# Optimization experiments

Measured on AMD Instinct MI355X. Metric: run time of the kernel, lower is better.

Reference implementation:

```python
import jax, jax.numpy as jnp
import numpy as np

N = 6144
D = 128
TAU = 0.1
ADJ_P = 0.005  # edge density


def _l2_normalize(x, eps=1e-12):
    # matches torch F.normalize: x / max(||x||, eps)
    n = jnp.sqrt(jnp.sum(x * x, axis=-1, keepdims=True))
    return x / jnp.maximum(n, eps)


def setup_inputs() -> dict:
    key = jax.random.key(0)
    ks = jax.random.split(key, 8)
    embF = jax.random.normal(ks[0], (N, D), jnp.float32)
    embM = jax.random.normal(ks[1], (N, D), jnp.float32)
    embP = jax.random.normal(ks[2], (N, D), jnp.float32)
    FM_adj = (jax.random.uniform(ks[3], (N, N)) < ADJ_P).astype(jnp.float32)
    FP_adj = (jax.random.uniform(ks[4], (N, N)) < ADJ_P).astype(jnp.float32)
    W1 = jax.random.normal(ks[5], (2 * D, D), jnp.float32) * (1.0 / np.sqrt(2 * D))
    b1 = jnp.zeros((D,), jnp.float32)
    W2 = jax.random.normal(ks[6], (D, 2), jnp.float32) * (1.0 / np.sqrt(D))
    b2 = jnp.zeros((2,), jnp.float32)
    return {"embF": embF, "embM": embM, "embP": embP,
            "FM_adj": FM_adj, "FP_adj": FP_adj,
            "W1": W1, "b1": b1, "W2": W2, "b2": b2}


def reference(embF, embM, embP, FM_adj, FP_adj, W1, b1, W2, b2):
    # attention-weighted neighbor aggregation
    FM_repr = (FM_adj @ embM) / jnp.maximum(FM_adj.sum(1, keepdims=True), 1.0)
    FP_repr = (FP_adj @ embP) / jnp.maximum(FP_adj.sum(1, keepdims=True), 1.0)
    # stack(dim=1).view(N,-1) == concat along feature dim
    feat = jnp.concatenate([FM_repr, FP_repr], axis=1)            # [N, 2D]
    h = jnp.maximum(feat @ W1 + b1, 0.0)                           # ReLU (dropout inactive in eval)
    weights = jax.nn.softmax(h @ W2 + b2, axis=-1)                 # [N, 2]

    Fn = _l2_normalize(embF)
    Mn = _l2_normalize(embM)
    Pn = _l2_normalize(embP)

    FM_sim = jnp.exp((Fn @ Mn.T) / TAU)                            # [N, Nm]
    FP_sim = jnp.exp((Fn @ Pn.T) / TAU)                            # [N, Np]

    FM_pos = jnp.sum(FM_sim * FM_adj, axis=1)
    FP_pos = jnp.sum(FP_sim * FP_adj, axis=1)
    FM_neg = jnp.sum(FM_sim, axis=1) - FM_pos
    FP_neg = jnp.sum(FP_sim, axis=1) - FP_pos

    w0, w1w = weights[:, 0], weights[:, 1]
    wp = w0 * FM_pos + w1w * FP_pos
    wn = w0 * FM_neg + w1w * FP_neg

    nei_count = jnp.maximum(FM_adj.sum(1) + FP_adj.sum(1), 1.0)
    ratio = wp / (wp + wn) / nei_count
    ratio = jnp.maximum(ratio, 1e-10)
    loss = jnp.mean(-jnp.log(ratio))
    return loss, weights
```

## Files before the change

### kernel.cpp

```cpp
#include <hip/hip_runtime.h>
#include <hip/hip_bf16.h>

#define NN 6144
#define DD 128
#define PBL 136
#define INV_TAU 10.0f

typedef __attribute__((ext_vector_type(4))) float f32x4;
typedef __attribute__((ext_vector_type(8))) short s16x8;

__global__ void k_normalize(const float* __restrict__ embF,
                            const float* __restrict__ embM,
                            const float* __restrict__ embP,
                            float* __restrict__ Fn,
                            float* __restrict__ rnM, float* __restrict__ rnP,
                            __hip_bfloat16* __restrict__ Fnb,
                            __hip_bfloat16* __restrict__ Mnb,
                            __hip_bfloat16* __restrict__ Pnb) {
    int which = blockIdx.y;
    const float* src = which == 0 ? embF : (which == 1 ? embM : embP);
    __hip_bfloat16* dstb = which == 0 ? Fnb : (which == 1 ? Mnb : Pnb);
    int wave = threadIdx.x >> 6, lane = threadIdx.x & 63;
    int row = blockIdx.x * 4 + wave;
    float2 v = reinterpret_cast<const float2*>(src + (size_t)row * DD)[lane];
    float s = v.x * v.x + v.y * v.y;
#pragma unroll
    for (int m = 1; m <= 32; m <<= 1) s += __shfl_xor(s, m);
    float inv = 1.0f / fmaxf(sqrtf(s), 1e-12f);
    float2 o; o.x = v.x * inv; o.y = v.y * inv;
    if (which == 0)
        reinterpret_cast<float2*>(Fn + (size_t)row * DD)[lane] = o;
    if (lane == 0) {
        if (which == 1) rnM[row] = inv;
        if (which == 2) rnP[row] = inv;
    }
    __hip_bfloat162 ob;
    ob.x = __float2bfloat16(o.x);
    ob.y = __float2bfloat16(o.y);
    reinterpret_cast<__hip_bfloat162*>(dstb + (size_t)row * DD)[lane] = ob;
}

__global__ __launch_bounds__(256) void k_scan(
        const float* __restrict__ FM_adj, const float* __restrict__ FP_adj,
        int* __restrict__ nzbuf, int* __restrict__ nzcnt,
        float* __restrict__ cntF, float* __restrict__ cntP) {
    __shared__ int lbuf[4][64 * 12];
    const int h = blockIdx.y;
    const float* adj = h ? FP_adj : FM_adj;
    const int w = threadIdx.x >> 6, lane = threadIdx.x & 63;
    const int row = blockIdx.x * 4 + w;
    const float4* rp = reinterpret_cast<const float4*>(adj + (size_t)row * NN);
    int* mybuf = &lbuf[w][lane * 12];
    int mycnt = 0;
    for (int b = 0; b < 3; ++b) {
        const int c0 = b * 8 * 64 + lane;
        float4 v0 = rp[c0];
        float4 v1 = rp[c0 + 64];
        float4 v2 = rp[c0 + 128];
        float4 v3 = rp[c0 + 192];
        float4 v4 = rp[c0 + 256];
        float4 v5 = rp[c0 + 320];
        float4 v6 = rp[c0 + 384];
        float4 v7 = rp[c0 + 448];
        float4 vv[8] = {v0, v1, v2, v3, v4, v5, v6, v7};
#pragma unroll
        for (int u = 0; u < 8; ++u) {
            int colbase = (b * 8 + u) * 256 + lane * 4;
            if (vv[u].x != 0.f) { if (mycnt < 12) mybuf[mycnt] = colbase;     mycnt++; }
            if (vv[u].y != 0.f) { if (mycnt < 12) mybuf[mycnt] = colbase + 1; mycnt++; }
            if (vv[u].z != 0.f) { if (mycnt < 12) mybuf[mycnt] = colbase + 2; mycnt++; }
            if (vv[u].w != 0.f) { if (mycnt < 12) mybuf[mycnt] = colbase + 3; mycnt++; }
        }
    }
    int cnt = mycnt < 12 ? mycnt : 12;
    int x = cnt;
#pragma unroll
    for (int d = 1; d < 64; d <<= 1) {
        int y = __shfl_up(x, d);
        if (lane >= d) x += y;
    }
    int pref = x - cnt;
    int totc = __shfl(x, 63);
    int t = mycnt;
#pragma unroll
    for (int msk = 1; msk <= 32; msk <<= 1) t += __shfl_xor(t, msk);
    const int base = (h * NN + row) << 7;
    for (int i = 0; i < cnt; ++i) {
        int slot = pref + i;
        if (slot < 128) nzbuf[base + slot] = mybuf[i];
    }
    if (lane == 0) {
        nzcnt[h * NN + row] = totc < 128 ? totc : 128;
        (h ? cntP : cntF)[row] = (float)t;
    }
}

__global__ __launch_bounds__(256) void k_dense(
        const __hip_bfloat16* __restrict__ Fnb,
        const __hip_bfloat16* __restrict__ Mnb,
        const __hip_bfloat16* __restrict__ Pnb,
        float* __restrict__ FMtot, float* __restrict__ FPtot) {
    __shared__ __hip_bfloat16 Bs[32][PBL];
    const int half = blockIdx.z;
    const __hip_bfloat16* Bnb = half ? Pnb : Mnb;
    float* TOT = half ? FPtot : FMtot;
    const int tid = threadIdx.x;
    const int w = tid >> 6, lane = tid & 63;
    const int m = lane & 15, q = lane >> 4;
    const int rb = blockIdx.x * 128 + w * 32;
    const int j0 = blockIdx.y * (NN / 8);
    const int srow = tid >> 4, scol = (tid & 15) * 8;

    s16x8 a[2][4];
#pragma unroll
    for (int g = 0; g < 2; ++g)
#pragma unroll
        for (int ks = 0; ks < 4; ++ks)
            a[g][ks] = *reinterpret_cast<const s16x8*>(
                Fnb + (size_t)(rb + g * 16 + m) * DD + ks * 32 + q * 8);

    const float4* gt0 = reinterpret_cast<const float4*>(Bnb + (size_t)j0 * DD);
    float4 s0 = gt0[tid], s1 = gt0[256 + tid];

    float tot[2][4] = {{0.f, 0.f, 0.f, 0.f}, {0.f, 0.f, 0.f, 0.f}};
    for (int it = 0; it < 24; ++it) {
        __syncthreads();
        *reinterpret_cast<float4*>(&Bs[srow][scol]) = s0;
        *reinterpret_cast<float4*>(&Bs[16 + srow][scol]) = s1;
        __syncthreads();
        if (it + 1 < 24) {
            const float4* gt = reinterpret_cast<const float4*>(
                Bnb + (size_t)(j0 + (it + 1) * 32) * DD);
            s0 = gt[tid];
            s1 = gt[256 + tid];
        }
        asm volatile("" ::: "memory");
        s16x8 b[2][4];
#pragma unroll
        for (int t = 0; t < 2; ++t)
#pragma unroll
            for (int ks = 0; ks < 4; ++ks)
                b[t][ks] = *reinterpret_cast<const s16x8*>(
                    &Bs[t * 16 + m][ks * 32 + q * 8]);
#pragma unroll
        for (int g = 0; g < 2; ++g)
#pragma unroll
            for (int t = 0; t < 2; ++t) {
                f32x4 acc = {0.f, 0.f, 0.f, 0.f};
#pragma unroll
                for (int ks = 0; ks < 4; ++ks)
                    acc = __builtin_amdgcn_mfma_f32_16x16x32_bf16(
                        a[g][ks], b[t][ks], acc, 0, 0, 0);
#pragma unroll
                for (int r = 0; r < 4; ++r)
                    tot[g][r] += __expf(acc[r] * INV_TAU);
            }
    }
#pragma unroll
    for (int msk = 1; msk <= 8; msk <<= 1)
#pragma unroll
        for (int g = 0; g < 2; ++g)
#pragma unroll
            for (int r = 0; r < 4; ++r)
                tot[g][r] += __shfl_xor(tot[g][r], msk);
    if (m == 0)
#pragma unroll
        for (int g = 0; g < 2; ++g)
#pragma unroll
            for (int r = 0; r < 4; ++r)
                atomicAdd(&TOT[rb + g * 16 + q * 4 + r], tot[g][r]);
}

__global__ void k_gather(const float* __restrict__ embM,
                         const float* __restrict__ embP,
                         const float* __restrict__ Fn,
                         const float* __restrict__ rnM,
                         const float* __restrict__ rnP,
                         const int* __restrict__ nzbuf,
                         const int* __restrict__ nzcnt,
                         const float* __restrict__ cntF,
                         const float* __restrict__ cntP,
                         float* __restrict__ feat,
                         float* __restrict__ FMpos, float* __restrict__ FPpos) {
    __shared__ int listS[128];
    __shared__ float rS[2][DD];
    __shared__ float posS[2];
    const int row = blockIdx.x, h = blockIdx.y;
    const int tid = threadIdx.x, wv = tid >> 6, lane = tid & 63;
    const float* embX = h ? embP : embM;
    const float* RN = h ? rnP : rnM;
    int K = nzcnt[h * NN + row];
    if (tid < K) listS[tid] = nzbuf[((h * NN + row) << 7) + tid];
    __syncthreads();
    float2 f = reinterpret_cast<const float2*>(Fn + (size_t)row * DD)[lane];
    float2 racc = {0.f, 0.f};
    float wsum = 0.f;
    for (int k = wv; k < K; k += 2) {
        int j = listS[k];
        float rn = RN[j];
        float2 e = reinterpret_cast<const float2*>(embX + (size_t)j * DD)[lane];
        racc.x += e.x;
        racc.y += e.y;
        float d = f.x * e.x + f.y * e.y;
#pragma unroll
        for (int msk = 1; msk <= 32; msk <<= 1) d += __shfl_xor(d, msk);
        wsum += __expf(d * rn * INV_TAU);
    }
    rS[wv][2 * lane] = racc.x;
    rS[wv][2 * lane + 1] = racc.y;
    if (lane == 0) posS[wv] = wsum;
    __syncthreads();
    float cn = (h ? cntP : cntF)[row];
    feat[(size_t)row * (2 * DD) + h * DD + tid] =
        (rS[0][tid] + rS[1][tid]) / fmaxf(cn, 1.0f);
    if (tid == 0) (h ? FPpos : FMpos)[row] = posS[0] + posS[1];
}

__global__ __launch_bounds__(256) void k_mlp(
        const float* __restrict__ feat,
        const float* __restrict__ W1, const float* __restrict__ b1,
        const float* __restrict__ W2, const float* __restrict__ b2,
        const float* __restrict__ FMpos, const float* __restrict__ FPpos,
        const float* __restrict__ FMtot, const float* __restrict__ FPtot,
        const float* __restrict__ cntF, const float* __restrict__ cntP,
        float* __restrict__ out) {
    __shared__ float featS[8][2 * DD];
    __shared__ float red[4][4][2];
    __shared__ float lossS[8];
    const int tid = threadIdx.x;
    const int g = tid >> 7, d = tid & 127;
    const int wv = tid >> 6, lane = tid & 63;
    const int row0 = blockIdx.x * 8;
    for (int idx = tid; idx < 8 * 2 * DD; idx += 256)
        featS[idx >> 8][idx & 255] = feat[(size_t)row0 * (2 * DD) + idx];
    __syncthreads();
    float bb = b1[d];
    float acc0 = bb, acc1 = bb, acc2 = bb, acc3 = bb;
    const float* fS = &featS[g * 4][0];
#pragma unroll 4
    for (int c = 0; c < 2 * DD; ++c) {
        float w1v = W1[c * DD + d];
        acc0 = fmaf(fS[0 * 256 + c], w1v, acc0);
        acc1 = fmaf(fS[1 * 256 + c], w1v, acc1);
        acc2 = fmaf(fS[2 * 256 + c], w1v, acc2);
        acc3 = fmaf(fS[3 * 256 + c], w1v, acc3);
    }
    float w20 = W2[2 * d], w21 = W2[2 * d + 1];
    float hr[4] = {fmaxf(acc0, 0.f), fmaxf(acc1, 0.f),
                   fmaxf(acc2, 0.f), fmaxf(acc3, 0.f)};
#pragma unroll
    for (int r = 0; r < 4; ++r) {
        float p0 = hr[r] * w20, p1 = hr[r] * w21;
#pragma unroll
        for (int msk = 1; msk <= 32; msk <<= 1) {
            p0 += __shfl_xor(p0, msk);
            p1 += __shfl_xor(p1, msk);
        }
        if (lane == 0) { red[wv][r][0] = p0; red[wv][r][1] = p1; }
    }
    __syncthreads();
    if (tid < 8) {
        int g2 = tid >> 2, r = tid & 3;
        int row = row0 + tid;
        float z0 = red[2 * g2][r][0] + red[2 * g2 + 1][r][0] + b2[0];
        float z1 = red[2 * g2][r][1] + red[2 * g2 + 1][r][1] + b2[1];
        float mx = fmaxf(z0, z1);
        float e0 = expf(z0 - mx), e1 = expf(z1 - mx);
        float inv = 1.0f / (e0 + e1);
        float w0 = e0 * inv, w1 = e1 * inv;
        out[1 + row * 2 + 0] = w0;
        out[1 + row * 2 + 1] = w1;
        float wp = w0 * FMpos[row] + w1 * FPpos[row];
        float wn = w0 * (FMtot[row] - FMpos[row]) +
                   w1 * (FPtot[row] - FPpos[row]);
        float nei = fmaxf(cntF[row] + cntP[row], 1.0f);
        float ratio = wp / (wp + wn) / nei;
        ratio = fmaxf(ratio, 1e-10f);
        lossS[tid] = -logf(ratio);
    }
    __syncthreads();
    if (tid == 0) {
        float L = 0.f;
#pragma unroll
        for (int r = 0; r < 8; ++r) L += lossS[r];
        atomicAdd(out, L * (1.0f / NN));
    }
}

extern "C" void kernel_launch(void* const* d_in, const int* in_sizes, int n_in,
                              void* d_out, int out_size, void* d_ws, size_t ws_size,
                              hipStream_t stream) {
    const float* embF   = (const float*)d_in[0];
    const float* embM   = (const float*)d_in[1];
    const float* embP   = (const float*)d_in[2];
    const float* FM_adj = (const float*)d_in[3];
    const float* FP_adj = (const float*)d_in[4];
    const float* W1     = (const float*)d_in[5];
    const float* b1     = (const float*)d_in[6];
    const float* W2     = (const float*)d_in[7];
    const float* b2     = (const float*)d_in[8];
    float* out = (float*)d_out;

    float* ws = (float*)d_ws;
    float* FMtot = ws;
    float* FPtot = FMtot + NN;
    float* FMpos = FPtot + NN;
    float* FPpos = FMpos + NN;
    float* cntF  = FPpos + NN;
    float* cntP  = cntF + NN;
    float* rnM   = cntP + NN;
    float* rnP   = rnM + NN;
    float* feat  = rnP + NN;
    float* Fn    = feat + (size_t)NN * 2 * DD;
    __hip_bfloat16* Fnb = (__hip_bfloat16*)(Fn + (size_t)NN * DD);
    __hip_bfloat16* Mnb = Fnb + (size_t)NN * DD;
    __hip_bfloat16* Pnb = Mnb + (size_t)NN * DD;
    int* nzbuf = (int*)(Pnb + (size_t)NN * DD);
    int* nzcnt = nzbuf + 2 * (size_t)NN * 128;

    hipMemsetAsync(FMtot, 0, 2 * NN * sizeof(float), stream);
    hipMemsetAsync(d_out, 0, sizeof(float), stream);

    k_normalize<<<dim3(NN / 4, 3), 256, 0, stream>>>(embF, embM, embP,
                                                     Fn, rnM, rnP,
                                                     Fnb, Mnb, Pnb);
    k_scan<<<dim3(NN / 4, 2), 256, 0, stream>>>(FM_adj, FP_adj,
                                                nzbuf, nzcnt, cntF, cntP);
    k_dense<<<dim3(NN / 128, 8, 2), 256, 0, stream>>>(Fnb, Mnb, Pnb,
                                                      FMtot, FPtot);
    k_gather<<<dim3(NN, 2), 128, 0, stream>>>(embM, embP, Fn, rnM, rnP,
                                              nzbuf, nzcnt, cntF, cntP,
                                              feat, FMpos, FPpos);
    k_mlp<<<dim3(NN / 8), 256, 0, stream>>>(feat, W1, b1, W2, b2,
                                            FMpos, FPpos, FMtot, FPtot,
                                            cntF, cntP, out);
}
```

Measured before the change: 449.9 us.

## Fuse adjacency scan with sparse gather, split dense grid finer, retile MLP

Merges the adjacency scan and the neighbor gather into one kernel with one block per row, so the nonzero index list stays in shared memory and the global nzbuf round trip and one launch go away. The dense similarity kernel's column split is doubled (16 chunks of 12 iterations) to give more blocks and parallelism, at the cost of more atomics. The MLP kernel is reorganised so each thread handles 8 rows over half the input channels, with a shared-memory reduction. Per-thread nonzero capacity drops from 12 to 4 entries, which relies on the sparse adjacency density.

```diff
diff --git a/kernel.cpp b/kernel.cpp
--- a/kernel.cpp
+++ b/kernel.cpp
@@ -40,58 +40,101 @@
     reinterpret_cast<__hip_bfloat162*>(dstb + (size_t)row * DD)[lane] = ob;
 }
 
-__global__ __launch_bounds__(256) void k_scan(
+__global__ __launch_bounds__(256) void k_sparse2(
         const float* __restrict__ FM_adj, const float* __restrict__ FP_adj,
-        int* __restrict__ nzbuf, int* __restrict__ nzcnt,
+        const float* __restrict__ embM, const float* __restrict__ embP,
+        const float* __restrict__ Fn,
+        const float* __restrict__ rnM, const float* __restrict__ rnP,
+        float* __restrict__ feat,
+        float* __restrict__ FMpos, float* __restrict__ FPpos,
         float* __restrict__ cntF, float* __restrict__ cntP) {
-    __shared__ int lbuf[4][64 * 12];
-    const int h = blockIdx.y;
-    const float* adj = h ? FP_adj : FM_adj;
-    const int w = threadIdx.x >> 6, lane = threadIdx.x & 63;
-    const int row = blockIdx.x * 4 + w;
+    __shared__ float FnS[DD];
+    __shared__ int lbufT[256][4];
+    __shared__ int listS[128];
+    __shared__ float reprS[8][DD];
+    __shared__ float posS[8];
+    __shared__ int wvS[4];
+    __shared__ int Ktot[2];
+    const int row = blockIdx.x, h = blockIdx.y;
+    const float* adj  = h ? FP_adj : FM_adj;
+    const float* embX = h ? embP : embM;
+    const float* RN   = h ? rnP : rnM;
+    const int tid = threadIdx.x, wv = tid >> 6, lane = tid & 63;
+
+    if (tid < 32)
+        reinterpret_cast<float4*>(FnS)[tid] =
+            reinterpret_cast<const float4*>(Fn + (size_t)row * DD)[tid];
+
     const float4* rp = reinterpret_cast<const float4*>(adj + (size_t)row * NN);
-    int* mybuf = &lbuf[w][lane * 12];
     int mycnt = 0;
-    for (int b = 0; b < 3; ++b) {
-        const int c0 = b * 8 * 64 + lane;
-        float4 v0 = rp[c0];
-        float4 v1 = rp[c0 + 64];
-        float4 v2 = rp[c0 + 128];
-        float4 v3 = rp[c0 + 192];
-        float4 v4 = rp[c0 + 256];
-        float4 v5 = rp[c0 + 320];
-        float4 v6 = rp[c0 + 384];
-        float4 v7 = rp[c0 + 448];
-        float4 vv[8] = {v0, v1, v2, v3, v4, v5, v6, v7};
-#pragma unroll
-        for (int u = 0; u < 8; ++u) {
-            int colbase = (b * 8 + u) * 256 + lane * 4;
-            if (vv[u].x != 0.f) { if (mycnt < 12) mybuf[mycnt] = colbase;     mycnt++; }
-            if (vv[u].y != 0.f) { if (mycnt < 12) mybuf[mycnt] = colbase + 1; mycnt++; }
-            if (vv[u].z != 0.f) { if (mycnt < 12) mybuf[mycnt] = colbase + 2; mycnt++; }
-            if (vv[u].w != 0.f) { if (mycnt < 12) mybuf[mycnt] = colbase + 3; mycnt++; }
-        }
-    }
-    int cnt = mycnt < 12 ? mycnt : 12;
+#pragma unroll
+    for (int it = 0; it < 6; ++it) {
+        float4 v = rp[it * 256 + tid];
+        int cb = (it * 256 + tid) * 4;
+        if (v.x != 0.f) { if (mycnt < 4) lbufT[tid][mycnt] = cb;     mycnt++; }
+        if (v.y != 0.f) { if (mycnt < 4) lbufT[tid][mycnt] = cb + 1; mycnt++; }
+        if (v.z != 0.f) { if (mycnt < 4) lbufT[tid][mycnt] = cb + 2; mycnt++; }
+        if (v.w != 0.f) { if (mycnt < 4) lbufT[tid][mycnt] = cb + 3; mycnt++; }
+    }
+    int cnt = mycnt < 4 ? mycnt : 4;
     int x = cnt;
 #pragma unroll
     for (int d = 1; d < 64; d <<= 1) {
         int y = __shfl_up(x, d);
         if (lane >= d) x += y;
     }
-    int pref = x - cnt;
-    int totc = __shfl(x, 63);
     int t = mycnt;
 #pragma unroll
     for (int msk = 1; msk <= 32; msk <<= 1) t += __shfl_xor(t, msk);
-    const int base = (h * NN + row) << 7;
+    if (tid == 0) Ktot[1] = 0;
+    if (lane == 63) wvS[wv] = x;
+    __syncthreads();
+    if (lane == 0) atomicAdd(&Ktot[1], t);
+    if (tid == 0) {
+        int s = 0;
+#pragma unroll
+        for (int i = 0; i < 4; ++i) { int v = wvS[i]; wvS[i] = s; s += v; }
+        Ktot[0] = s < 128 ? s : 128;
+    }
+    __syncthreads();
+    int off = wvS[wv] + (x - cnt);
     for (int i = 0; i < cnt; ++i) {
-        int slot = pref + i;
-        if (slot < 128) nzbuf[base + slot] = mybuf[i];
-    }
-    if (lane == 0) {
-        nzcnt[h * NN + row] = totc < 128 ? totc : 128;
-        (h ? cntP : cntF)[row] = (float)t;
+        int s = off + i;
+        if (s < 128) listS[s] = lbufT[tid][i];
+    }
+    __syncthreads();
+    const int K = Ktot[0];
+    const float trueK = (float)Ktot[1];
+
+    const int hw = tid >> 5, sl = tid & 31;
+    float4 f4 = reinterpret_cast<const float4*>(FnS)[sl];
+    float4 racc = {0.f, 0.f, 0.f, 0.f};
+    float wsum = 0.f;
+    for (int k = hw; k < K; k += 8) {
+        int j = listS[k];
+        float rn = RN[j];
+        float4 e = reinterpret_cast<const float4*>(embX + (size_t)j * DD)[sl];
+        racc.x += e.x; racc.y += e.y; racc.z += e.z; racc.w += e.w;
+        float d = f4.x * e.x + f4.y * e.y + f4.z * e.z + f4.w * e.w;
+#pragma unroll
+        for (int msk = 1; msk <= 16; msk <<= 1) d += __shfl_xor(d, msk);
+        wsum += __expf(d * rn * INV_TAU);
+    }
+    reinterpret_cast<float4*>(&reprS[hw][0])[sl] = racc;
+    if (sl == 0) posS[hw] = wsum;
+    __syncthreads();
+    if (tid < DD) {
+        float s = 0.f;
+#pragma unroll
+        for (int i = 0; i < 8; ++i) s += reprS[i][tid];
+        feat[(size_t)row * (2 * DD) + h * DD + tid] = s / fmaxf(trueK, 1.0f);
+    }
+    if (tid == 0) {
+        float p = 0.f;
+#pragma unroll
+        for (int i = 0; i < 8; ++i) p += posS[i];
+        (h ? FPpos : FMpos)[row] = p;
+        (h ? cntP : cntF)[row] = trueK;
     }
 }
 
@@ -108,7 +151,7 @@
     const int w = tid >> 6, lane = tid & 63;
     const int m = lane & 15, q = lane >> 4;
     const int rb = blockIdx.x * 128 + w * 32;
-    const int j0 = blockIdx.y * (NN / 8);
+    const int j0 = blockIdx.y * (NN / 16);
     const int srow = tid >> 4, scol = (tid & 15) * 8;
 
     s16x8 a[2][4];
@@ -123,12 +166,12 @@
     float4 s0 = gt0[tid], s1 = gt0[256 + tid];
 
     float tot[2][4] = {{0.f, 0.f, 0.f, 0.f}, {0.f, 0.f, 0.f, 0.f}};
-    for (int it = 0; it < 24; ++it) {
+    for (int it = 0; it < 12; ++it) {
         __syncthreads();
         *reinterpret_cast<float4*>(&Bs[srow][scol]) = s0;
         *reinterpret_cast<float4*>(&Bs[16 + srow][scol]) = s1;
         __syncthreads();
-        if (it + 1 < 24) {
+        if (it + 1 < 12) {
             const float4* gt = reinterpret_cast<const float4*>(
                 Bnb + (size_t)(j0 + (it + 1) * 32) * DD);
             s0 = gt[tid];
@@ -169,51 +212,6 @@
 #pragma unroll
             for (int r = 0; r < 4; ++r)
                 atomicAdd(&TOT[rb + g * 16 + q * 4 + r], tot[g][r]);
-}
-
-__global__ void k_gather(const float* __restrict__ embM,
-                         const float* __restrict__ embP,
-                         const float* __restrict__ Fn,
-                         const float* __restrict__ rnM,
-                         const float* __restrict__ rnP,
-                         const int* __restrict__ nzbuf,
-                         const int* __restrict__ nzcnt,
-                         const float* __restrict__ cntF,
-                         const float* __restrict__ cntP,
-                         float* __restrict__ feat,
-                         float* __restrict__ FMpos, float* __restrict__ FPpos) {
-    __shared__ int listS[128];
-    __shared__ float rS[2][DD];
-    __shared__ float posS[2];
-    const int row = blockIdx.x, h = blockIdx.y;
-    const int tid = threadIdx.x, wv = tid >> 6, lane = tid & 63;
-    const float* embX = h ? embP : embM;
-    const float* RN = h ? rnP : rnM;
-    int K = nzcnt[h * NN + row];
-    if (tid < K) listS[tid] = nzbuf[((h * NN + row) << 7) + tid];
-    __syncthreads();
-    float2 f = reinterpret_cast<const float2*>(Fn + (size_t)row * DD)[lane];
-    float2 racc = {0.f, 0.f};
-    float wsum = 0.f;
-    for (int k = wv; k < K; k += 2) {
-        int j = listS[k];
-        float rn = RN[j];
-        float2 e = reinterpret_cast<const float2*>(embX + (size_t)j * DD)[lane];
-        racc.x += e.x;
-        racc.y += e.y;
-        float d = f.x * e.x + f.y * e.y;
-#pragma unroll
-        for (int msk = 1; msk <= 32; msk <<= 1) d += __shfl_xor(d, msk);
-        wsum += __expf(d * rn * INV_TAU);
-    }
-    rS[wv][2 * lane] = racc.x;
-    rS[wv][2 * lane + 1] = racc.y;
-    if (lane == 0) posS[wv] = wsum;
-    __syncthreads();
-    float cn = (h ? cntP : cntF)[row];
-    feat[(size_t)row * (2 * DD) + h * DD + tid] =
-        (rS[0][tid] + rS[1][tid]) / fmaxf(cn, 1.0f);
-    if (tid == 0) (h ? FPpos : FMpos)[row] = posS[0] + posS[1];
 }
 
 __global__ __launch_bounds__(256) void k_mlp(
@@ -225,45 +223,59 @@
         const float* __restrict__ cntF, const float* __restrict__ cntP,
         float* __restrict__ out) {
     __shared__ float featS[8][2 * DD];
-    __shared__ float red[4][4][2];
+    __shared__ float partS[2][8][DD];
+    __shared__ float redS[2][8][2];
     __shared__ float lossS[8];
     const int tid = threadIdx.x;
-    const int g = tid >> 7, d = tid & 127;
-    const int wv = tid >> 6, lane = tid & 63;
+    const int cp = tid >> 7, d = tid & 127;
     const int row0 = blockIdx.x * 8;
     for (int idx = tid; idx < 8 * 2 * DD; idx += 256)
         featS[idx >> 8][idx & 255] = feat[(size_t)row0 * (2 * DD) + idx];
     __syncthreads();
-    float bb = b1[d];
-    float acc0 = bb, acc1 = bb, acc2 = bb, acc3 = bb;
-    const float* fS = &featS[g * 4][0];
-#pragma unroll 4
-    for (int c = 0; c < 2 * DD; ++c) {
-        float w1v = W1[c * DD + d];
-        acc0 = fmaf(fS[0 * 256 + c], w1v, acc0);
-        acc1 = fmaf(fS[1 * 256 + c], w1v, acc1);
-        acc2 = fmaf(fS[2 * 256 + c], w1v, acc2);
-        acc3 = fmaf(fS[3 * 256 + c], w1v, acc3);
-    }
-    float w20 = W2[2 * d], w21 = W2[2 * d + 1];
-    float hr[4] = {fmaxf(acc0, 0.f), fmaxf(acc1, 0.f),
-                   fmaxf(acc2, 0.f), fmaxf(acc3, 0.f)};
-#pragma unroll
-    for (int r = 0; r < 4; ++r) {
-        float p0 = hr[r] * w20, p1 = hr[r] * w21;
-#pragma unroll
-        for (int msk = 1; msk <= 32; msk <<= 1) {
-            p0 += __shfl_xor(p0, msk);
-            p1 += __shfl_xor(p1, msk);
+    float bb = (cp == 0) ? b1[d] : 0.f;
+    float acc[8];
+#pragma unroll
+    for (int r = 0; r < 8; ++r) acc[r] = bb;
+    const int c0 = cp * 128;
+    for (int c = c0; c < c0 + 128; c += 2) {
+        float wA = W1[c * DD + d];
+        float wB = W1[(c + 1) * DD + d];
+#pragma unroll
+        for (int r = 0; r < 8; ++r)
+            acc[r] = fmaf(featS[r][c + 1], wB, fmaf(featS[r][c], wA, acc[r]));
+    }
+#pragma unroll
+    for (int r = 0; r < 8; ++r) partS[cp][r][d] = acc[r];
+    __syncthreads();
+    if (tid < 128) {
+        const int lane = tid & 63, wv = tid >> 6;
+        float w20 = W2[2 * tid], w21 = W2[2 * tid + 1];
+        float p0s[8], p1s[8];
+#pragma unroll
+        for (int r = 0; r < 8; ++r) {
+            float hh = fmaxf(partS[0][r][tid] + partS[1][r][tid], 0.f);
+            p0s[r] = hh * w20;
+            p1s[r] = hh * w21;
         }
-        if (lane == 0) { red[wv][r][0] = p0; red[wv][r][1] = p1; }
+#pragma unroll
+        for (int r = 0; r < 8; ++r)
+#pragma unroll
+            for (int msk = 1; msk <= 32; msk <<= 1) {
+                p0s[r] += __shfl_xor(p0s[r], msk);
+                p1s[r] += __shfl_xor(p1s[r], msk);
+            }
+        if (lane == 0)
+#pragma unroll
+            for (int r = 0; r < 8; ++r) {
+                redS[wv][r][0] = p0s[r];
+                redS[wv][r][1] = p1s[r];
+            }
     }
     __syncthreads();
     if (tid < 8) {
-        int g2 = tid >> 2, r = tid & 3;
         int row = row0 + tid;
-        float z0 = red[2 * g2][r][0] + red[2 * g2 + 1][r][0] + b2[0];
-        float z1 = red[2 * g2][r][1] + red[2 * g2 + 1][r][1] + b2[1];
+        float z0 = redS[0][tid][0] + redS[1][tid][0] + b2[0];
+        float z1 = redS[0][tid][1] + redS[1][tid][1] + b2[1];
         float mx = fmaxf(z0, z1);
         float e0 = expf(z0 - mx), e1 = expf(z1 - mx);
         float inv = 1.0f / (e0 + e1);
@@ -315,8 +327,6 @@
     __hip_bfloat16* Fnb = (__hip_bfloat16*)(Fn + (size_t)NN * DD);
     __hip_bfloat16* Mnb = Fnb + (size_t)NN * DD;
     __hip_bfloat16* Pnb = Mnb + (size_t)NN * DD;
-    int* nzbuf = (int*)(Pnb + (size_t)NN * DD);
-    int* nzcnt = nzbuf + 2 * (size_t)NN * 128;
 
     hipMemsetAsync(FMtot, 0, 2 * NN * sizeof(float), stream);
     hipMemsetAsync(d_out, 0, sizeof(float), stream);
@@ -324,13 +334,11 @@
     k_normalize<<<dim3(NN / 4, 3), 256, 0, stream>>>(embF, embM, embP,
                                                      Fn, rnM, rnP,
                                                      Fnb, Mnb, Pnb);
-    k_scan<<<dim3(NN / 4, 2), 256, 0, stream>>>(FM_adj, FP_adj,
-                                                nzbuf, nzcnt, cntF, cntP);
-    k_dense<<<dim3(NN / 128, 8, 2), 256, 0, stream>>>(Fnb, Mnb, Pnb,
-                                                      FMtot, FPtot);
-    k_gather<<<dim3(NN, 2), 128, 0, stream>>>(embM, embP, Fn, rnM, rnP,
-                                              nzbuf, nzcnt, cntF, cntP,
-                                              feat, FMpos, FPpos);
+    k_sparse2<<<dim3(NN, 2), 256, 0, stream>>>(FM_adj, FP_adj, embM, embP,
+                                               Fn, rnM, rnP, feat,
+                                               FMpos, FPpos, cntF, cntP);
+    k_dense<<<dim3(NN / 128, 16, 2), 256, 0, stream>>>(Fnb, Mnb, Pnb,
+                                                       FMtot, FPtot);
     k_mlp<<<dim3(NN / 8), 256, 0, stream>>>(feat, W1, b1, W2, b2,
                                             FMpos, FPpos, FMtot, FPtot,
                                             cntF, cntP, out);
```

After: 391.7 us. 12.9% less time.
